# Performance work log

Measured on AMD Instinct MI355X. Metric: run time of the kernel, lower is better.

The kernel has to match this reference:

```python
import jax, jax.numpy as jnp
import numpy as np

# dims: B scenes, V views, T tokens per view, D=d1=d2 embed dim, H=4*D mlp hidden
B, V, T, D = 2, 8, 512, 1024
H = 4 * D
LN_EPS = 1e-5


def setup_inputs() -> dict:
    key = jax.random.key(0)
    ks = jax.random.split(key, 9)
    x = jax.random.normal(ks[0], (B, V, T, D), jnp.float32)
    theta_Q = jax.random.normal(ks[1], (D, D), jnp.float32)  # Task.theta_Q ~ randn
    # TTT_MLP params (nn.Linear default-init scale approximated; exact dist irrelevant for math)
    W1 = jax.random.normal(ks[2], (D, H), jnp.float32) * (1.0 / np.sqrt(D))
    b1 = jnp.zeros((H,), jnp.float32)
    W2 = jax.random.normal(ks[3], (H, D), jnp.float32) * (1.0 / np.sqrt(H))
    b2 = jnp.zeros((D,), jnp.float32)
    gamma = jnp.ones((D,), jnp.float32)   # LayerNorm weight
    beta = jnp.zeros((D,), jnp.float32)   # LayerNorm bias
    alpha = jnp.full((1, D), 0.01, jnp.float32)
    return {"x": x, "theta_Q": theta_Q, "W1": W1, "b1": b1, "W2": W2,
            "b2": b2, "gamma": gamma, "beta": beta, "alpha": alpha}


def _layernorm(y, gamma, beta):
    mu = jnp.mean(y, axis=-1, keepdims=True)
    var = jnp.mean(jnp.square(y - mu), axis=-1, keepdims=True)  # biased, as torch LayerNorm
    return (y - mu) * jax.lax.rsqrt(var + LN_EPS) * gamma + beta


def reference(x, theta_Q, W1, b1, W2, b2, gamma, beta, alpha):
    # NOTE: in the original module, update_model rebinds a local (`p = p - lr*g`),
    # so the learner params are NEVER updated; proxy_loss/grads are dead code w.r.t.
    # the output. Faithful math: out = TTT_MLP(x @ theta_Q), fully parallel over tokens.
    z = jnp.einsum('bvtd,de->bvte', x, theta_Q)          # [B,V,T,D]
    h = jax.nn.gelu(z @ W1 + b1, approximate=False)      # exact erf GELU, as torch nn.GELU
    y = h @ W2 + b2                                      # [B,V,T,D]
    ln = _layernorm(y, gamma, beta)
    return z + jnp.tanh(alpha) * ln
```

## Files before the change

### kernel.cpp

```cpp
#include <hip/hip_runtime.h>
#include <hip/hip_bf16.h>
#include <cstdint>
#include <math.h>

typedef __hip_bfloat16 bf16_t;
typedef __attribute__((ext_vector_type(8))) __bf16 bf16x8;
typedef __attribute__((ext_vector_type(4))) float f32x4;

static_assert(sizeof(bf16x8) == 16, "bf16x8 must be 4 VGPRs");

static constexpr int DD = 1024;
static constexpr int HH = 4096;

#define GLD16(gp, lp)                                                                              \
  __builtin_amdgcn_global_load_lds(                                                                \
      (__attribute__((address_space(1))) void*)(uintptr_t)(gp),                                    \
      (__attribute__((address_space(3))) void*)(uint32_t)(uintptr_t)(lp), 16, 0, 0)

#if !__has_builtin(__builtin_amdgcn_exp2f)
#define __builtin_amdgcn_exp2f(x) exp2f(x)
#endif
#if !__has_builtin(__builtin_amdgcn_rcpf)
#define __builtin_amdgcn_rcpf(x) (1.0f / (x))
#endif

__device__ __forceinline__ float fast_gelu(float u) {
  const float t = __builtin_amdgcn_exp2f(-2.4554089f * u);
  return u * __builtin_amdgcn_rcpf(1.0f + t);
}

__global__ __launch_bounds__(256) void k_split_x(const float* __restrict__ x,
                                                 bf16_t* __restrict__ xh,
                                                 bf16_t* __restrict__ xl, int n4) {
  int i = blockIdx.x * 256 + threadIdx.x;
  const int stride = gridDim.x * 256;
  for (; i < n4; i += stride) {
    const float4 v = reinterpret_cast<const float4*>(x)[i];
    float vv[4] = {v.x, v.y, v.z, v.w};
    union { bf16_t b[4]; short4 s; } H, L;
#pragma unroll
    for (int j = 0; j < 4; ++j) {
      H.b[j] = __float2bfloat16(vv[j]);
      L.b[j] = __float2bfloat16(vv[j] - __bfloat162float(H.b[j]));
    }
    reinterpret_cast<short4*>(xh)[i] = H.s;
    reinterpret_cast<short4*>(xl)[i] = L.s;
  }
}

template <bool SPLIT>
__global__ __launch_bounds__(256) void k_transpose(const float* __restrict__ W,
                                                   bf16_t* __restrict__ Th,
                                                   bf16_t* __restrict__ Tl, int K, int N) {
  __shared__ float tile[32][33];
  const int n0 = blockIdx.x * 32, k0 = blockIdx.y * 32;
  const int tx = threadIdx.x, ty = threadIdx.y;
#pragma unroll
  for (int r = 0; r < 4; ++r) {
    const int k = ty + r * 8;
    tile[k][tx] = W[(size_t)(k0 + k) * N + n0 + tx];
  }
  __syncthreads();
#pragma unroll
  for (int r = 0; r < 4; ++r) {
    const int n = ty + r * 8;
    const float v = tile[tx][n];
    const bf16_t h = __float2bfloat16(v);
    Th[(size_t)(n0 + n) * K + k0 + tx] = h;
    if (SPLIT) Tl[(size_t)(n0 + n) * K + k0 + tx] = __float2bfloat16(v - __bfloat162float(h));
  }
}

__global__ __launch_bounds__(256) void k_gemm_split(const bf16_t* __restrict__ Ah,
                                                    const bf16_t* __restrict__ Al,
                                                    const bf16_t* __restrict__ BTh,
                                                    const bf16_t* __restrict__ BTl,
                                                    float* __restrict__ Cf,
                                                    bf16_t* __restrict__ Cb,
                                                    int M, int N, int K) {
  constexpr int BM = 128, BN = 128, BK = 32;
  __shared__ __align__(16) bf16_t sAh[BM * BK];
  __shared__ __align__(16) bf16_t sBh[BN * BK];
  __shared__ __align__(16) bf16_t sAl[BM * BK];
  __shared__ __align__(16) bf16_t sBl[BN * BK];

  const int nbn = N / BN;
  const int nwg = gridDim.x;
  const int wg = blockIdx.x;
  const int cpx = nwg >> 3;
  const int swz = (wg & 7) * cpx + (wg >> 3);
  const int bm = swz / nbn, bn = swz % nbn;

  const int t = threadIdx.x;
  const int l = t & 63;
  const int w = t >> 6;
  const int wr = (w >> 1) * 64, wc = (w & 1) * 64;

  const size_t Abase = (size_t)bm * BM * K;
  const size_t Bbase = (size_t)bn * BN * K;

  const int r0 = t >> 2, kc0 = (t & 3) * 8;
  const int r1 = r0 + 64;

  f32x4 acc[4][4] = {};
  const int lm = l & 15;
  const int l4 = l >> 4;
  const int kb8 = l4 * 8;

  const int nk = K / BK;
  for (int kt = 0; kt < nk; ++kt) {
    const size_t gk = (size_t)kt * BK;
    GLD16(Ah + Abase + (size_t)r0 * K + gk + kc0, &sAh[r0 * BK + kc0]);
    GLD16(Ah + Abase + (size_t)r1 * K + gk + kc0, &sAh[r1 * BK + kc0]);
    GLD16(BTh + Bbase + (size_t)r0 * K + gk + kc0, &sBh[r0 * BK + kc0]);
    GLD16(BTh + Bbase + (size_t)r1 * K + gk + kc0, &sBh[r1 * BK + kc0]);
    GLD16(Al + Abase + (size_t)r0 * K + gk + kc0, &sAl[r0 * BK + kc0]);
    GLD16(Al + Abase + (size_t)r1 * K + gk + kc0, &sAl[r1 * BK + kc0]);
    GLD16(BTl + Bbase + (size_t)r0 * K + gk + kc0, &sBl[r0 * BK + kc0]);
    GLD16(BTl + Bbase + (size_t)r1 * K + gk + kc0, &sBl[r1 * BK + kc0]);
    __syncthreads();

    bf16x8 a[4], b[4];
#pragma unroll
    for (int m = 0; m < 4; ++m)
      a[m] = *reinterpret_cast<const bf16x8*>(&sAh[(wr + m * 16 + lm) * BK + kb8]);
#pragma unroll
    for (int n = 0; n < 4; ++n)
      b[n] = *reinterpret_cast<const bf16x8*>(&sBh[(wc + n * 16 + lm) * BK + kb8]);
#pragma unroll
    for (int m = 0; m < 4; ++m)
#pragma unroll
      for (int n = 0; n < 4; ++n)
        acc[m][n] = __builtin_amdgcn_mfma_f32_16x16x32_bf16(a[m], b[n], acc[m][n], 0, 0, 0);

    {
      bf16x8 al_[4], bl_[4];
#pragma unroll
      for (int m = 0; m < 4; ++m)
        al_[m] = *reinterpret_cast<const bf16x8*>(&sAl[(wr + m * 16 + lm) * BK + kb8]);
#pragma unroll
      for (int n = 0; n < 4; ++n)
        bl_[n] = *reinterpret_cast<const bf16x8*>(&sBl[(wc + n * 16 + lm) * BK + kb8]);
#pragma unroll
      for (int m = 0; m < 4; ++m)
#pragma unroll
        for (int n = 0; n < 4; ++n) {
          acc[m][n] = __builtin_amdgcn_mfma_f32_16x16x32_bf16(a[m], bl_[n], acc[m][n], 0, 0, 0);
          acc[m][n] = __builtin_amdgcn_mfma_f32_16x16x32_bf16(al_[m], b[n], acc[m][n], 0, 0, 0);
        }
    }
    __syncthreads();
  }

  const int cr = l4 * 4;
#pragma unroll
  for (int m = 0; m < 4; ++m) {
#pragma unroll
    for (int n = 0; n < 4; ++n) {
      const int c = bn * BN + wc + n * 16 + lm;
#pragma unroll
      for (int j = 0; j < 4; ++j) {
        const int r = bm * BM + wr + m * 16 + cr + j;
        const size_t idx = (size_t)r * N + c;
        const float v = acc[m][n][j];
        Cf[idx] = v;
        Cb[idx] = __float2bfloat16(v);
      }
    }
  }
}

template <int EPI>
__global__ __launch_bounds__(256) void k_gemm_pipe(const bf16_t* __restrict__ A,
                                                   const bf16_t* __restrict__ BT,
                                                   const float* __restrict__ bias,
                                                   float* __restrict__ Cf,
                                                   bf16_t* __restrict__ Cb,
                                                   int M, int N, int K, int LDK) {
  constexpr int BM = 128, BN = 128, BK = 64;
  __shared__ __align__(16) bf16_t sA[2][BM * BK];
  __shared__ __align__(16) bf16_t sB[2][BN * BK];

  const int nbn = N / BN;
  const int nwg = gridDim.x;
  const int wg = blockIdx.x;
  const int cpx = nwg >> 3;
  const int swz = (wg & 7) * cpx + (wg >> 3);
  const int bm = swz / nbn, bn = swz % nbn;

  const int ks = blockIdx.y;
  const size_t k0 = (size_t)ks * K;
  Cf += (size_t)ks * M * N;

  const int t = threadIdx.x;
  const int l = t & 63;
  const int w = t >> 6;
  const int wr = (w >> 1) * 64, wc = (w & 1) * 64;

  const size_t Abase = (size_t)bm * BM * LDK + k0;
  const size_t Bbase = (size_t)bn * BN * LDK + k0;

  const int lm = l & 15;
  const int l4 = l >> 4;

  auto stage = [&](int kt, int pb) {
    const size_t gk = (size_t)kt * BK;
#pragma unroll
    for (int p = 0; p < 4; ++p) {
      const int c = t + 256 * p;
      const int r = c >> 3, j = c & 7;
      const int jg = (j ^ (r & 7)) * 8;
      GLD16(A + Abase + (size_t)r * LDK + gk + jg, &sA[pb][c * 8]);
    }
#pragma unroll
    for (int p = 0; p < 4; ++p) {
      const int c = t + 256 * p;
      const int r = c >> 3, j = c & 7;
      const int jg = (j ^ (r & 7)) * 8;
      GLD16(BT + Bbase + (size_t)r * LDK + gk + jg, &sB[pb][c * 8]);
    }
  };

  f32x4 acc[4][4] = {};
  const int nk = K / BK;

  stage(0, 0);
  stage(1, 1);
  for (int kt = 0; kt < nk; ++kt) {
    const int pb = kt & 1;
    if (kt + 1 < nk) {
      asm volatile("s_waitcnt vmcnt(8)" ::: "memory");
    } else {
      asm volatile("s_waitcnt vmcnt(0)" ::: "memory");
    }
    __builtin_amdgcn_s_barrier();
    __builtin_amdgcn_sched_barrier(0);

#pragma unroll
    for (int h = 0; h < 2; ++h) {
      bf16x8 a[4], b[4];
#pragma unroll
      for (int m = 0; m < 4; ++m) {
        const int R = wr + m * 16 + lm;
        const int q = (l4 + 4 * h) ^ (R & 7);
        a[m] = *reinterpret_cast<const bf16x8*>(&sA[pb][R * 64 + q * 8]);
      }
#pragma unroll
      for (int n = 0; n < 4; ++n) {
        const int R = wc + n * 16 + lm;
        const int q = (l4 + 4 * h) ^ (R & 7);
        b[n] = *reinterpret_cast<const bf16x8*>(&sB[pb][R * 64 + q * 8]);
      }
#pragma unroll
      for (int m = 0; m < 4; ++m)
#pragma unroll
        for (int n = 0; n < 4; ++n)
          acc[m][n] = __builtin_amdgcn_mfma_f32_16x16x32_bf16(a[m], b[n], acc[m][n], 0, 0, 0);
    }

    __builtin_amdgcn_sched_barrier(0);
    __builtin_amdgcn_s_barrier();
    if (kt + 2 < nk) stage(kt + 2, pb);
  }

  const int cr = l4 * 4;
#pragma unroll
  for (int m = 0; m < 4; ++m) {
#pragma unroll
    for (int n = 0; n < 4; ++n) {
      const int c = bn * BN + wc + n * 16 + lm;
      const float bc = (EPI == 2) ? bias[c] : 0.0f;
#pragma unroll
      for (int j = 0; j < 4; ++j) {
        const int r = bm * BM + wr + m * 16 + cr + j;
        const size_t idx = (size_t)r * N + c;
        const float v = acc[m][n][j];
        if (EPI == 2) {
          Cb[idx] = __float2bfloat16(fast_gelu(v + bc));
        } else {
          Cf[idx] = v;
        }
      }
    }
  }
}

__global__ __launch_bounds__(256) void k_ln_res(const float* __restrict__ y0,
                                                const float* __restrict__ y1,
                                                const float* __restrict__ b2,
                                                const float* __restrict__ z,
                                                const float* __restrict__ gamma,
                                                const float* __restrict__ beta,
                                                const float* __restrict__ alpha,
                                                float* __restrict__ out) {
  const int row = blockIdx.x;
  const int t = threadIdx.x;
  const float4 va = reinterpret_cast<const float4*>(y0 + (size_t)row * DD)[t];
  const float4 vb = reinterpret_cast<const float4*>(y1 + (size_t)row * DD)[t];
  const float4 bc = reinterpret_cast<const float4*>(b2)[t];
  float4 v;
  v.x = va.x + vb.x + bc.x; v.y = va.y + vb.y + bc.y;
  v.z = va.z + vb.z + bc.z; v.w = va.w + vb.w + bc.w;
  float s = v.x + v.y + v.z + v.w;
  float q = v.x * v.x + v.y * v.y + v.z * v.z + v.w * v.w;
#pragma unroll
  for (int m = 1; m < 64; m <<= 1) {
    s += __shfl_xor(s, m, 64);
    q += __shfl_xor(q, m, 64);
  }
  __shared__ float ss[4], sq[4];
  if ((t & 63) == 0) { ss[t >> 6] = s; sq[t >> 6] = q; }
  __syncthreads();
  s = ss[0] + ss[1] + ss[2] + ss[3];
  q = sq[0] + sq[1] + sq[2] + sq[3];
  const float mu = s * (1.0f / DD);
  const float var = fmaxf(q * (1.0f / DD) - mu * mu, 0.0f);
  const float rs = rsqrtf(var + 1e-5f);
  const float4 g = reinterpret_cast<const float4*>(gamma)[t];
  const float4 bb = reinterpret_cast<const float4*>(beta)[t];
  const float4 aa = reinterpret_cast<const float4*>(alpha)[t];
  const float4 zz = reinterpret_cast<const float4*>(z + (size_t)row * DD)[t];
  float4 o;
  o.x = zz.x + tanhf(aa.x) * ((v.x - mu) * rs * g.x + bb.x);
  o.y = zz.y + tanhf(aa.y) * ((v.y - mu) * rs * g.y + bb.y);
  o.z = zz.z + tanhf(aa.z) * ((v.z - mu) * rs * g.z + bb.z);
  o.w = zz.w + tanhf(aa.w) * ((v.w - mu) * rs * g.w + bb.w);
  reinterpret_cast<float4*>(out + (size_t)row * DD)[t] = o;
}

extern "C" void kernel_launch(void* const* d_in, const int* in_sizes, int n_in, void* d_out,
                              int out_size, void* d_ws, size_t ws_size, hipStream_t stream) {
  const float* x   = (const float*)d_in[0];
  const float* thQ = (const float*)d_in[1];
  const float* W1  = (const float*)d_in[2];
  const float* b1  = (const float*)d_in[3];
  const float* W2  = (const float*)d_in[4];
  const float* b2  = (const float*)d_in[5];
  const float* gam = (const float*)d_in[6];
  const float* bet = (const float*)d_in[7];
  const float* alp = (const float*)d_in[8];
  float* out = (float*)d_out;

  const int M = in_sizes[0] / DD;

  char* ws = (char*)d_ws;
  size_t off = 0;
  auto take = [&](size_t bytes) -> char* {
    char* p = ws + off;
    off += (bytes + 255) & ~(size_t)255;
    return p;
  };
  bf16_t* xh  = (bf16_t*)take((size_t)M * DD * 2);
  bf16_t* xl  = (bf16_t*)take((size_t)M * DD * 2);
  bf16_t* qTh = (bf16_t*)take((size_t)DD * DD * 2);
  bf16_t* qTl = (bf16_t*)take((size_t)DD * DD * 2);
  bf16_t* w1T = (bf16_t*)take((size_t)DD * HH * 2);
  bf16_t* w2T = (bf16_t*)take((size_t)HH * DD * 2);
  float*  zf  = (float*)take((size_t)M * DD * 4);
  bf16_t* zb  = (bf16_t*)take((size_t)M * DD * 2);
  bf16_t* hb  = (bf16_t*)take((size_t)M * HH * 2);
  float*  yf  = (float*)take((size_t)M * DD * 4 * 2);

  hipLaunchKernelGGL(k_split_x, dim3(2048), dim3(256), 0, stream, x, xh, xl, M * DD / 4);
  hipLaunchKernelGGL((k_transpose<true>), dim3(DD / 32, DD / 32), dim3(32, 8), 0, stream,
                     thQ, qTh, qTl, DD, DD);
  hipLaunchKernelGGL((k_transpose<false>), dim3(HH / 32, DD / 32), dim3(32, 8), 0, stream,
                     W1, w1T, (bf16_t*)nullptr, DD, HH);
  hipLaunchKernelGGL((k_transpose<false>), dim3(DD / 32, HH / 32), dim3(32, 8), 0, stream,
                     W2, w2T, (bf16_t*)nullptr, HH, DD);

  hipLaunchKernelGGL(k_gemm_split, dim3((M / 128) * (DD / 128)), dim3(256), 0, stream,
                     xh, xl, qTh, qTl, zf, zb, M, DD, DD);
  hipLaunchKernelGGL((k_gemm_pipe<2>), dim3((M / 128) * (HH / 128)), dim3(256), 0, stream,
                     zb, w1T, b1, (float*)nullptr, hb, M, HH, DD, DD);
  hipLaunchKernelGGL((k_gemm_pipe<3>), dim3((M / 128) * (DD / 128), 2), dim3(256), 0, stream,
                     hb, w2T, (const float*)nullptr, yf, (bf16_t*)nullptr, M, DD, HH / 2, HH);
  hipLaunchKernelGGL(k_ln_res, dim3(M), dim3(256), 0, stream,
                     yf, yf + (size_t)M * DD, b2, zf, gam, bet, alp, out);
}
```

Baseline: 364.0 us.

## Enlarge MLP GEMM tiles to 256x256 with 8 waves and split compute phases

Replaces the 128x128x64 pipelined GEMM used for the two MLP matmuls with a 256x256x32 tile kernel run by 512 threads (8 waves, each computing 128x64). Each wave's work is split into two halves separated by a barrier, with explicit LDS waits and raised wave priority around the MFMA blocks. The larger tile is meant to raise arithmetic intensity and cut global/LDS traffic per FLOP. In exchange it uses more accumulator registers, launches fewer workgroups (a concern for the second GEMM with only 32x2 blocks), and shortens the K step, which adds more barriers per unit of work.

```diff
diff --git a/kernel.cpp b/kernel.cpp
--- a/kernel.cpp
+++ b/kernel.cpp
@@ -171,13 +171,13 @@
 }
 
 template <int EPI>
-__global__ __launch_bounds__(256) void k_gemm_pipe(const bf16_t* __restrict__ A,
-                                                   const bf16_t* __restrict__ BT,
-                                                   const float* __restrict__ bias,
-                                                   float* __restrict__ Cf,
-                                                   bf16_t* __restrict__ Cb,
-                                                   int M, int N, int K, int LDK) {
-  constexpr int BM = 128, BN = 128, BK = 64;
+__global__ __launch_bounds__(512, 2) void k_gemm_256(const bf16_t* __restrict__ A,
+                                                     const bf16_t* __restrict__ BT,
+                                                     const float* __restrict__ bias,
+                                                     float* __restrict__ Cf,
+                                                     bf16_t* __restrict__ Cb,
+                                                     int M, int N, int K, int LDK) {
+  constexpr int BM = 256, BN = 256, BK = 32;
   __shared__ __align__(16) bf16_t sA[2][BM * BK];
   __shared__ __align__(16) bf16_t sB[2][BN * BK];
 
@@ -195,7 +195,8 @@
   const int t = threadIdx.x;
   const int l = t & 63;
   const int w = t >> 6;
-  const int wr = (w >> 1) * 64, wc = (w & 1) * 64;
+  const int wr = (w >> 2) * 128;
+  const int wc = (w & 3) * 64;
 
   const size_t Abase = (size_t)bm * BM * LDK + k0;
   const size_t Bbase = (size_t)bn * BN * LDK + k0;
@@ -206,22 +207,22 @@
   auto stage = [&](int kt, int pb) {
     const size_t gk = (size_t)kt * BK;
 #pragma unroll
-    for (int p = 0; p < 4; ++p) {
-      const int c = t + 256 * p;
-      const int r = c >> 3, j = c & 7;
-      const int jg = (j ^ (r & 7)) * 8;
+    for (int p = 0; p < 2; ++p) {
+      const int c = t + 512 * p;
+      const int r = c >> 2, j = c & 3;
+      const int jg = (j ^ (r & 3)) * 8;
       GLD16(A + Abase + (size_t)r * LDK + gk + jg, &sA[pb][c * 8]);
     }
 #pragma unroll
-    for (int p = 0; p < 4; ++p) {
-      const int c = t + 256 * p;
-      const int r = c >> 3, j = c & 7;
-      const int jg = (j ^ (r & 7)) * 8;
+    for (int p = 0; p < 2; ++p) {
+      const int c = t + 512 * p;
+      const int r = c >> 2, j = c & 3;
+      const int jg = (j ^ (r & 3)) * 8;
       GLD16(BT + Bbase + (size_t)r * LDK + gk + jg, &sB[pb][c * 8]);
     }
   };
 
-  f32x4 acc[4][4] = {};
+  f32x4 acc[8][4] = {};
   const int nk = K / BK;
 
   stage(0, 0);
@@ -229,35 +230,57 @@
   for (int kt = 0; kt < nk; ++kt) {
     const int pb = kt & 1;
     if (kt + 1 < nk) {
-      asm volatile("s_waitcnt vmcnt(8)" ::: "memory");
+      asm volatile("s_waitcnt vmcnt(4)" ::: "memory");
     } else {
       asm volatile("s_waitcnt vmcnt(0)" ::: "memory");
     }
     __builtin_amdgcn_s_barrier();
     __builtin_amdgcn_sched_barrier(0);
 
-#pragma unroll
-    for (int h = 0; h < 2; ++h) {
-      bf16x8 a[4], b[4];
+    bf16x8 b[4];
+#pragma unroll
+    for (int n = 0; n < 4; ++n) {
+      const int R = wc + n * 16 + lm;
+      const int q = l4 ^ (R & 3);
+      b[n] = *reinterpret_cast<const bf16x8*>(&sB[pb][R * BK + q * 8]);
+    }
+    {
+      bf16x8 a[4];
 #pragma unroll
       for (int m = 0; m < 4; ++m) {
         const int R = wr + m * 16 + lm;
-        const int q = (l4 + 4 * h) ^ (R & 7);
-        a[m] = *reinterpret_cast<const bf16x8*>(&sA[pb][R * 64 + q * 8]);
+        const int q = l4 ^ (R & 3);
+        a[m] = *reinterpret_cast<const bf16x8*>(&sA[pb][R * BK + q * 8]);
       }
-#pragma unroll
-      for (int n = 0; n < 4; ++n) {
-        const int R = wc + n * 16 + lm;
-        const int q = (l4 + 4 * h) ^ (R & 7);
-        b[n] = *reinterpret_cast<const bf16x8*>(&sB[pb][R * 64 + q * 8]);
-      }
+      asm volatile("s_waitcnt lgkmcnt(0)" ::: "memory");
+      __builtin_amdgcn_sched_barrier(0);
+      __builtin_amdgcn_s_setprio(1);
 #pragma unroll
       for (int m = 0; m < 4; ++m)
 #pragma unroll
         for (int n = 0; n < 4; ++n)
           acc[m][n] = __builtin_amdgcn_mfma_f32_16x16x32_bf16(a[m], b[n], acc[m][n], 0, 0, 0);
-    }
-
+      __builtin_amdgcn_s_setprio(0);
+    }
+    __builtin_amdgcn_s_barrier();
+    {
+      bf16x8 a[4];
+#pragma unroll
+      for (int m = 0; m < 4; ++m) {
+        const int R = wr + 64 + m * 16 + lm;
+        const int q = l4 ^ (R & 3);
+        a[m] = *reinterpret_cast<const bf16x8*>(&sA[pb][R * BK + q * 8]);
+      }
+      asm volatile("s_waitcnt lgkmcnt(0)" ::: "memory");
+      __builtin_amdgcn_sched_barrier(0);
+      __builtin_amdgcn_s_setprio(1);
+#pragma unroll
+      for (int m = 0; m < 4; ++m)
+#pragma unroll
+        for (int n = 0; n < 4; ++n)
+          acc[4 + m][n] = __builtin_amdgcn_mfma_f32_16x16x32_bf16(a[m], b[n], acc[4 + m][n], 0, 0, 0);
+      __builtin_amdgcn_s_setprio(0);
+    }
     __builtin_amdgcn_sched_barrier(0);
     __builtin_amdgcn_s_barrier();
     if (kt + 2 < nk) stage(kt + 2, pb);
@@ -265,14 +288,15 @@
 
   const int cr = l4 * 4;
 #pragma unroll
-  for (int m = 0; m < 4; ++m) {
+  for (int m = 0; m < 8; ++m) {
+    const int rbase = bm * BM + wr + ((m < 4) ? m * 16 : 64 + (m - 4) * 16);
 #pragma unroll
     for (int n = 0; n < 4; ++n) {
       const int c = bn * BN + wc + n * 16 + lm;
       const float bc = (EPI == 2) ? bias[c] : 0.0f;
 #pragma unroll
       for (int j = 0; j < 4; ++j) {
-        const int r = bm * BM + wr + m * 16 + cr + j;
+        const int r = rbase + cr + j;
         const size_t idx = (size_t)r * N + c;
         const float v = acc[m][n][j];
         if (EPI == 2) {
@@ -371,9 +395,9 @@
 
   hipLaunchKernelGGL(k_gemm_split, dim3((M / 128) * (DD / 128)), dim3(256), 0, stream,
                      xh, xl, qTh, qTl, zf, zb, M, DD, DD);
-  hipLaunchKernelGGL((k_gemm_pipe<2>), dim3((M / 128) * (HH / 128)), dim3(256), 0, stream,
+  hipLaunchKernelGGL((k_gemm_256<2>), dim3((M / 256) * (HH / 256)), dim3(512), 0, stream,
                      zb, w1T, b1, (float*)nullptr, hb, M, HH, DD, DD);
-  hipLaunchKernelGGL((k_gemm_pipe<3>), dim3((M / 128) * (DD / 128), 2), dim3(256), 0, stream,
+  hipLaunchKernelGGL((k_gemm_256<3>), dim3((M / 256) * (DD / 256), 2), dim3(512), 0, stream,
                      hb, w2T, (const float*)nullptr, yf, (bf16_t*)nullptr, M, DD, HH / 2, HH);
   hipLaunchKernelGGL(k_ln_res, dim3(M), dim3(256), 0, stream,
                      yf, yf + (size_t)M * DD, b2, zf, gam, bet, alp, out);
```

After: 360.8 us. No clear change (-0.9%).
